# Optimization experiments

Measured on AMD Instinct MI355X. Metric: run time of the kernel, lower is better.

The kernel has to match this reference:

```python
import jax, jax.numpy as jnp
import numpy as np

NUM_EXPERTS_PER_TOK = 2

def setup_inputs() -> dict:
    key = jax.random.key(0)
    k1, k2, k3, k4 = jax.random.split(key, 4)
    B, S, D, O, E = 2, 4096, 2048, 2048, 8
    x = jax.random.normal(k1, (B, S, D), dtype=jnp.float32)
    gate_w = jax.random.normal(k2, (E, D), dtype=jnp.float32) * 0.02
    expert_w = jax.random.normal(k3, (E, O, D), dtype=jnp.float32) * 0.02
    expert_b = jax.random.normal(k4, (E, O), dtype=jnp.float32) * 0.02
    return {"x": x, "gate_w": gate_w, "expert_w": expert_w, "expert_b": expert_b}

def reference(x, gate_w, expert_w, expert_b):
    E = gate_w.shape[0]
    O = expert_w.shape[1]
    # Router: gate logits [B,S,E], top-k selection, softmax over the k logits (fp32 then cast)
    gate_logits = jnp.einsum('bsd,ed->bse', x, gate_w)
    topk_vals, topk_idx = jax.lax.top_k(gate_logits, NUM_EXPERTS_PER_TOK)
    weights = jax.nn.softmax(topk_vals.astype(jnp.float32), axis=-1).astype(x.dtype)
    # Dense combine weights [B,S,E]: weight of expert e for each token (0 if not selected)
    dense_w = jnp.sum(jax.nn.one_hot(topk_idx, E, dtype=x.dtype) * weights[..., None], axis=2)
    # Per-expert linear + weighted combine (loop over small fixed E)
    out = jnp.zeros(x.shape[:2] + (O,), dtype=x.dtype)
    for e in range(E):
        y_e = jnp.einsum('bsd,od->bso', x, expert_w[e]) + expert_b[e]
        out = out + dense_w[..., e:e + 1] * y_e
    return out
```

## Files before the change

kernel.cpp:

```cpp
#include <hip/hip_runtime.h>
#include <stdint.h>
#include <math.h>

#define T_TOK 8192
#define DIM   2048
#define OUTD  2048
#define NEXP  8

typedef __bf16 bf16x8 __attribute__((ext_vector_type(8)));
typedef float  f32x4  __attribute__((ext_vector_type(4)));

__device__ __forceinline__ unsigned short f2bf(float f) {
  union { float f; uint32_t u; } c = {f};
  uint32_t r = (c.u + 0x7FFFu + ((c.u >> 16) & 1u)) >> 16;
  return (unsigned short)r;
}
__device__ __forceinline__ float bf2f(unsigned short h) {
  union { uint32_t u; float f; } c = {((uint32_t)h) << 16};
  return c.f;
}

__device__ __forceinline__ void gld_lds16(const void* g, void* l) {
  auto gp = reinterpret_cast<const __attribute__((address_space(1))) char*>(
      reinterpret_cast<uintptr_t>(g));
  auto lp = reinterpret_cast<__attribute__((address_space(3))) char*>(
      reinterpret_cast<uintptr_t>(l));
  __builtin_amdgcn_global_load_lds(gp, lp, 16, 0, 0);
}

__global__ __launch_bounds__(256) void split_hi_lo(const float* __restrict__ src,
                                                   unsigned short* __restrict__ hi,
                                                   unsigned short* __restrict__ lo,
                                                   int n4) {
  int stride = gridDim.x * blockDim.x;
  for (int i = blockIdx.x * blockDim.x + threadIdx.x; i < n4; i += stride) {
    float4 v = reinterpret_cast<const float4*>(src)[i];
    ushort4 h, l;
    h.x = f2bf(v.x); l.x = f2bf(v.x - bf2f(h.x));
    h.y = f2bf(v.y); l.y = f2bf(v.y - bf2f(h.y));
    h.z = f2bf(v.z); l.z = f2bf(v.z - bf2f(h.z));
    h.w = f2bf(v.w); l.w = f2bf(v.w - bf2f(h.w));
    reinterpret_cast<ushort4*>(hi)[i] = h;
    reinterpret_cast<ushort4*>(lo)[i] = l;
  }
}

__global__ __launch_bounds__(256) void router(const float* __restrict__ x,
                                              const float* __restrict__ gw,
                                              int* __restrict__ cnt,
                                              int* __restrict__ tok_list,
                                              float* __restrict__ tok_w) {
  const int t    = blockIdx.x * 4 + (threadIdx.x >> 6);
  const int lane = threadIdx.x & 63;
  const float4* xr = reinterpret_cast<const float4*>(x + (size_t)t * DIM);
  double acc[NEXP];
#pragma unroll
  for (int e = 0; e < NEXP; ++e) acc[e] = 0.0;
#pragma unroll
  for (int i = 0; i < DIM / (4 * 64); ++i) {
    float4 xv = xr[i * 64 + lane];
#pragma unroll
    for (int e = 0; e < NEXP; ++e) {
      float4 gv = reinterpret_cast<const float4*>(gw + e * DIM)[i * 64 + lane];
      acc[e] += (double)xv.x * gv.x + (double)xv.y * gv.y +
                (double)xv.z * gv.z + (double)xv.w * gv.w;
    }
  }
#pragma unroll
  for (int off = 32; off >= 1; off >>= 1)
#pragma unroll
    for (int e = 0; e < NEXP; ++e) acc[e] += __shfl_down(acc[e], off, 64);
  if (lane == 0) {
    float lg[NEXP];
#pragma unroll
    for (int e = 0; e < NEXP; ++e) lg[e] = (float)acc[e];
    int i0 = 0; float v0 = lg[0];
    int i1 = -1; float v1 = -3.4e38f;
#pragma unroll
    for (int e = 1; e < NEXP; ++e) {
      if (lg[e] > v0)      { i1 = i0; v1 = v0; i0 = e; v0 = lg[e]; }
      else if (lg[e] > v1) { i1 = e;  v1 = lg[e]; }
    }
    float p  = expf(v1 - v0);
    float w0 = 1.0f / (1.0f + p);
    float w1 = p * w0;
    int s0 = atomicAdd(&cnt[i0], 1);
    tok_list[i0 * T_TOK + s0] = t; tok_w[i0 * T_TOK + s0] = w0;
    int s1 = atomicAdd(&cnt[i1], 1);
    tok_list[i1 * T_TOK + s1] = t; tok_w[i1 * T_TOK + s1] = w1;
  }
}

__global__ __launch_bounds__(256, 2) void moe_gemm(
    const unsigned short* __restrict__ xh, const unsigned short* __restrict__ xl,
    const unsigned short* __restrict__ wh, const unsigned short* __restrict__ wl,
    const float* __restrict__ eb,
    const int* __restrict__ cnt,
    const int* __restrict__ tok_list, const float* __restrict__ tok_w,
    float* __restrict__ out) {
  const int e  = blockIdx.z;
  const int ce = cnt[e];
  const int bx = blockIdx.x;
  if (bx * 128 >= ce) return;
  const int by  = blockIdx.y;
  const int tid = threadIdx.x;
  const int l   = tid & 63;
  const int w   = tid >> 6;
  const int wr  = w >> 1, wc = w & 1;

  extern __shared__ char smem[];

  int* stok = reinterpret_cast<int*>(smem);
  if (tid < 128) {
    int rg = bx * 128 + tid;
    stok[tid] = (rg < ce) ? tok_list[e * T_TOK + rg] : 0;
  }
  __syncthreads();

  size_t aOff[4], bOff[4];
  int    lOff[4];
#pragma unroll
  for (int i = 0; i < 4; ++i) {
    int g = i * 256 + tid;
    int r = g >> 3, p = g & 7, s = p ^ (r & 7);
    aOff[i] = (size_t)stok[r] * DIM + s * 8;
    bOff[i] = ((size_t)e * OUTD + by * 128 + r) * DIM + s * 8;
    lOff[i] = g * 16;
  }
  __syncthreads();

  const int rA = wr * 64 + (l & 15);
  const int rB = wc * 64 + (l & 15);
  const int p0 = ((l >> 4) + 0) ^ (l & 7);
  const int p1 = ((l >> 4) + 4) ^ (l & 7);
  const int a0 = rA * 128 + p0 * 16, a1 = rA * 128 + p1 * 16;
  const int b0 = rB * 128 + p0 * 16, b1 = rB * 128 + p1 * 16;

  f32x4 acc[4][4] = {};

  for (int kt = 0; kt < DIM / 64; ++kt) {
    const int kk = kt * 64;
#pragma unroll
    for (int i = 0; i < 4; ++i) {
      gld_lds16(xh + aOff[i] + kk, smem +         lOff[i]);
      gld_lds16(xl + aOff[i] + kk, smem + 16384 + lOff[i]);
      gld_lds16(wh + bOff[i] + kk, smem + 32768 + lOff[i]);
      gld_lds16(wl + bOff[i] + kk, smem + 49152 + lOff[i]);
    }
    asm volatile("s_waitcnt vmcnt(0)" ::: "memory");
    __syncthreads();

#pragma unroll
    for (int ks = 0; ks < 2; ++ks) {
      const int aB = ks ? a1 : a0;
      const int bB = ks ? b1 : b0;
      bf16x8 ah[4], al[4];
#pragma unroll
      for (int m = 0; m < 4; ++m) {
        ah[m] = *reinterpret_cast<const bf16x8*>(smem +         aB + m * 2048);
        al[m] = *reinterpret_cast<const bf16x8*>(smem + 16384 + aB + m * 2048);
      }
#pragma unroll
      for (int n = 0; n < 4; ++n) {
        bf16x8 bh = *reinterpret_cast<const bf16x8*>(smem + 32768 + bB + n * 2048);
        bf16x8 bl = *reinterpret_cast<const bf16x8*>(smem + 49152 + bB + n * 2048);
#pragma unroll
        for (int m = 0; m < 4; ++m) {
          acc[m][n] = __builtin_amdgcn_mfma_f32_16x16x32_bf16(ah[m], bh, acc[m][n], 0, 0, 0);
          acc[m][n] = __builtin_amdgcn_mfma_f32_16x16x32_bf16(ah[m], bl, acc[m][n], 0, 0, 0);
          acc[m][n] = __builtin_amdgcn_mfma_f32_16x16x32_bf16(al[m], bh, acc[m][n], 0, 0, 0);
        }
      }
    }
    __syncthreads();
  }

  int   tk[16];
  float wt[16];
  const int q4 = (l >> 4) * 4;
#pragma unroll
  for (int m = 0; m < 4; ++m)
#pragma unroll
    for (int q = 0; q < 4; ++q) {
      int r  = wr * 64 + m * 16 + q4 + q;
      int rg = bx * 128 + r;
      bool v = rg < ce;
      tk[m * 4 + q] = v ? tok_list[e * T_TOK + rg] : 0;
      wt[m * 4 + q] = v ? tok_w[e * T_TOK + rg] : 0.0f;
    }
#pragma unroll
  for (int n = 0; n < 4; ++n) {
    const int gc = by * 128 + wc * 64 + n * 16 + (l & 15);
    const float bias = eb[e * OUTD + gc];
#pragma unroll
    for (int m = 0; m < 4; ++m)
#pragma unroll
      for (int q = 0; q < 4; ++q) {
        float val = wt[m * 4 + q] * (acc[m][n][q] + bias);
        atomicAdd(out + (size_t)tk[m * 4 + q] * OUTD + gc, val);
      }
  }
}

extern "C" void kernel_launch(void* const* d_in, const int* in_sizes, int n_in,
                              void* d_out, int out_size, void* d_ws, size_t ws_size,
                              hipStream_t stream) {
  const float* x  = (const float*)d_in[0];
  const float* gw = (const float*)d_in[1];
  const float* ew = (const float*)d_in[2];
  const float* eb = (const float*)d_in[3];
  float* out = (float*)d_out;

  char* ws = (char*)d_ws;
  int*   cnt      = (int*)(ws);
  int*   tok_list = (int*)(ws + 256);
  float* tok_w    = (float*)(ws + 256 + 262144);
  unsigned short* xh = (unsigned short*)(ws + 524544);
  unsigned short* xl = xh + 16777216;
  unsigned short* wh = xl + 16777216;
  unsigned short* wl = wh + 33554432;

  hipMemsetAsync(cnt, 0, 256, stream);
  hipMemsetAsync(d_out, 0, (size_t)out_size * sizeof(float), stream);

  split_hi_lo<<<4096, 256, 0, stream>>>(x,  xh, xl, 16777216 / 4);
  split_hi_lo<<<4096, 256, 0, stream>>>(ew, wh, wl, 33554432 / 4);
  router<<<T_TOK / 4, 256, 0, stream>>>(x, gw, cnt, tok_list, tok_w);

  moe_gemm<<<dim3(64, 16, 8), 256, 65536, stream>>>(xh, xl, wh, wl, eb, cnt,
                                                    tok_list, tok_w, out);
}
```

Before: 1.260 ms.

## Double-buffer MoE GEMM with 256x256 tiles and fuse x split into router

Fuses the hi/lo bf16 split of x into the router kernel so x is read once instead of twice. Restructures the expert GEMM to 512-thread blocks on 256x256 output tiles with a 32-wide K step and double-buffered LDS (133 KB), issuing the next stage's global->LDS loads before computing the current one. Token ids and weights are cached in LDS for the epilogue. The larger tile improves data reuse and the prefetch overlaps memory with MFMA, but it raises LDS and register pressure, likely limits occupancy to one block per CU, and pads more rows for experts with ragged token counts.

```diff
diff --git a/kernel.cpp b/kernel.cpp
--- a/kernel.cpp
+++ b/kernel.cpp
@@ -6,6 +6,7 @@
 #define DIM   2048
 #define OUTD  2048
 #define NEXP  8
+#define NKT   (DIM / 32)
 
 typedef __bf16 bf16x8 __attribute__((ext_vector_type(8)));
 typedef float  f32x4  __attribute__((ext_vector_type(4)));
@@ -45,20 +46,31 @@
   }
 }
 
-__global__ __launch_bounds__(256) void router(const float* __restrict__ x,
-                                              const float* __restrict__ gw,
-                                              int* __restrict__ cnt,
-                                              int* __restrict__ tok_list,
-                                              float* __restrict__ tok_w) {
+__global__ __launch_bounds__(256) void router_split(const float* __restrict__ x,
+                                                    const float* __restrict__ gw,
+                                                    unsigned short* __restrict__ xh,
+                                                    unsigned short* __restrict__ xl,
+                                                    int* __restrict__ cnt,
+                                                    int* __restrict__ tok_list,
+                                                    float* __restrict__ tok_w) {
   const int t    = blockIdx.x * 4 + (threadIdx.x >> 6);
   const int lane = threadIdx.x & 63;
   const float4* xr = reinterpret_cast<const float4*>(x + (size_t)t * DIM);
+  ushort4* xhr = reinterpret_cast<ushort4*>(xh + (size_t)t * DIM);
+  ushort4* xlr = reinterpret_cast<ushort4*>(xl + (size_t)t * DIM);
   double acc[NEXP];
 #pragma unroll
   for (int e = 0; e < NEXP; ++e) acc[e] = 0.0;
 #pragma unroll
   for (int i = 0; i < DIM / (4 * 64); ++i) {
     float4 xv = xr[i * 64 + lane];
+    ushort4 h, l;
+    h.x = f2bf(xv.x); l.x = f2bf(xv.x - bf2f(h.x));
+    h.y = f2bf(xv.y); l.y = f2bf(xv.y - bf2f(h.y));
+    h.z = f2bf(xv.z); l.z = f2bf(xv.z - bf2f(h.z));
+    h.w = f2bf(xv.w); l.w = f2bf(xv.w - bf2f(h.w));
+    xhr[i * 64 + lane] = h;
+    xlr[i * 64 + lane] = l;
 #pragma unroll
     for (int e = 0; e < NEXP; ++e) {
       float4 gv = reinterpret_cast<const float4*>(gw + e * DIM)[i * 64 + lane];
@@ -91,7 +103,7 @@
   }
 }
 
-__global__ __launch_bounds__(256, 2) void moe_gemm(
+__global__ __launch_bounds__(512, 2) void moe_gemm(
     const unsigned short* __restrict__ xh, const unsigned short* __restrict__ xl,
     const unsigned short* __restrict__ wh, const unsigned short* __restrict__ wl,
     const float* __restrict__ eb,
@@ -101,105 +113,104 @@
   const int e  = blockIdx.z;
   const int ce = cnt[e];
   const int bx = blockIdx.x;
-  if (bx * 128 >= ce) return;
+  if (bx * 256 >= ce) return;
   const int by  = blockIdx.y;
   const int tid = threadIdx.x;
   const int l   = tid & 63;
   const int w   = tid >> 6;
-  const int wr  = w >> 1, wc = w & 1;
+  const int wr  = w >> 2, wc = w & 3;
 
   extern __shared__ char smem[];
-
-  int* stok = reinterpret_cast<int*>(smem);
-  if (tid < 128) {
-    int rg = bx * 128 + tid;
-    stok[tid] = (rg < ce) ? tok_list[e * T_TOK + rg] : 0;
+  int*   stok = reinterpret_cast<int*>(smem + 131072);
+  float* sw   = reinterpret_cast<float*>(smem + 132096);
+
+  if (tid < 256) {
+    int rg = bx * 256 + tid;
+    bool v = rg < ce;
+    stok[tid] = v ? tok_list[e * T_TOK + rg] : 0;
+    sw[tid]   = v ? tok_w[e * T_TOK + rg]   : 0.0f;
   }
   __syncthreads();
 
-  size_t aOff[4], bOff[4];
-  int    lOff[4];
+  const unsigned short* asrc[4];
+  const unsigned short* bsrc[4];
 #pragma unroll
   for (int i = 0; i < 4; ++i) {
-    int g = i * 256 + tid;
+    int g = i * 512 + tid;
     int r = g >> 3, p = g & 7, s = p ^ (r & 7);
-    aOff[i] = (size_t)stok[r] * DIM + s * 8;
-    bOff[i] = ((size_t)e * OUTD + by * 128 + r) * DIM + s * 8;
-    lOff[i] = g * 16;
-  }
+    asrc[i] = (s < 4 ? xh : xl) + (size_t)stok[r] * DIM + (s & 3) * 8;
+    bsrc[i] = (s < 4 ? wh : wl) + ((size_t)e * OUTD + by * 256 + r) * DIM + (s & 3) * 8;
+  }
+
+  const int ph = (l >> 4) ^ (l & 7);
+  const int pl = ((l >> 4) + 4) ^ (l & 7);
+  const int aOh = (wr * 128 + (l & 15)) * 128 + ph * 16;
+  const int aOl = (wr * 128 + (l & 15)) * 128 + pl * 16;
+  const int bOh = 32768 + (wc * 64 + (l & 15)) * 128 + ph * 16;
+  const int bOl = 32768 + (wc * 64 + (l & 15)) * 128 + pl * 16;
+
+  f32x4 acc[8][4] = {};
+
+  auto STAGE = [&](int buf, int kk) {
+    char* base = smem + buf * 65536;
+#pragma unroll
+    for (int i = 0; i < 4; ++i) {
+      gld_lds16(asrc[i] + kk, base + tid * 16 + i * 8192);
+      gld_lds16(bsrc[i] + kk, base + 32768 + tid * 16 + i * 8192);
+    }
+  };
+
+  STAGE(0, 0);
+  asm volatile("s_waitcnt vmcnt(0)" ::: "memory");
   __syncthreads();
 
-  const int rA = wr * 64 + (l & 15);
-  const int rB = wc * 64 + (l & 15);
-  const int p0 = ((l >> 4) + 0) ^ (l & 7);
-  const int p1 = ((l >> 4) + 4) ^ (l & 7);
-  const int a0 = rA * 128 + p0 * 16, a1 = rA * 128 + p1 * 16;
-  const int b0 = rB * 128 + p0 * 16, b1 = rB * 128 + p1 * 16;
-
-  f32x4 acc[4][4] = {};
-
-  for (int kt = 0; kt < DIM / 64; ++kt) {
-    const int kk = kt * 64;
-#pragma unroll
-    for (int i = 0; i < 4; ++i) {
-      gld_lds16(xh + aOff[i] + kk, smem +         lOff[i]);
-      gld_lds16(xl + aOff[i] + kk, smem + 16384 + lOff[i]);
-      gld_lds16(wh + bOff[i] + kk, smem + 32768 + lOff[i]);
-      gld_lds16(wl + bOff[i] + kk, smem + 49152 + lOff[i]);
+  for (int kt = 0; kt < NKT; ++kt) {
+    const int cur = kt & 1;
+    if (kt + 1 < NKT) STAGE(cur ^ 1, (kt + 1) * 32);
+
+    char* b = smem + cur * 65536;
+    bf16x8 bh[4], bl[4];
+#pragma unroll
+    for (int n = 0; n < 4; ++n) {
+      bh[n] = *reinterpret_cast<const bf16x8*>(b + bOh + n * 2048);
+      bl[n] = *reinterpret_cast<const bf16x8*>(b + bOl + n * 2048);
+    }
+#pragma unroll
+    for (int m = 0; m < 8; ++m) {
+      bf16x8 ah = *reinterpret_cast<const bf16x8*>(b + aOh + m * 2048);
+      bf16x8 al = *reinterpret_cast<const bf16x8*>(b + aOl + m * 2048);
+#pragma unroll
+      for (int n = 0; n < 4; ++n) {
+        acc[m][n] = __builtin_amdgcn_mfma_f32_16x16x32_bf16(ah, bh[n], acc[m][n], 0, 0, 0);
+        acc[m][n] = __builtin_amdgcn_mfma_f32_16x16x32_bf16(ah, bl[n], acc[m][n], 0, 0, 0);
+        acc[m][n] = __builtin_amdgcn_mfma_f32_16x16x32_bf16(al, bh[n], acc[m][n], 0, 0, 0);
+      }
     }
     asm volatile("s_waitcnt vmcnt(0)" ::: "memory");
     __syncthreads();
-
-#pragma unroll
-    for (int ks = 0; ks < 2; ++ks) {
-      const int aB = ks ? a1 : a0;
-      const int bB = ks ? b1 : b0;
-      bf16x8 ah[4], al[4];
-#pragma unroll
-      for (int m = 0; m < 4; ++m) {
-        ah[m] = *reinterpret_cast<const bf16x8*>(smem +         aB + m * 2048);
-        al[m] = *reinterpret_cast<const bf16x8*>(smem + 16384 + aB + m * 2048);
+  }
+
+#pragma unroll
+  for (int n = 0; n < 4; ++n) {
+    const int gc = by * 256 + wc * 64 + n * 16 + (l & 15);
+    const float bias = eb[e * OUTD + gc];
+#pragma unroll
+    for (int m = 0; m < 8; ++m) {
+      const int r = wr * 128 + m * 16 + (l >> 4) * 4;
+#pragma unroll
+      for (int q = 0; q < 4; ++q) {
+        int   tk = stok[r + q];
+        float wt = sw[r + q];
+        float val = wt * (acc[m][n][q] + bias);
+        atomicAdd(out + (size_t)tk * OUTD + gc, val);
       }
-#pragma unroll
-      for (int n = 0; n < 4; ++n) {
-        bf16x8 bh = *reinterpret_cast<const bf16x8*>(smem + 32768 + bB + n * 2048);
-        bf16x8 bl = *reinterpret_cast<const bf16x8*>(smem + 49152 + bB + n * 2048);
-#pragma unroll
-        for (int m = 0; m < 4; ++m) {
-          acc[m][n] = __builtin_amdgcn_mfma_f32_16x16x32_bf16(ah[m], bh, acc[m][n], 0, 0, 0);
-          acc[m][n] = __builtin_amdgcn_mfma_f32_16x16x32_bf16(ah[m], bl, acc[m][n], 0, 0, 0);
-          acc[m][n] = __builtin_amdgcn_mfma_f32_16x16x32_bf16(al[m], bh, acc[m][n], 0, 0, 0);
-        }
-      }
-    }
-    __syncthreads();
-  }
-
-  int   tk[16];
-  float wt[16];
-  const int q4 = (l >> 4) * 4;
-#pragma unroll
-  for (int m = 0; m < 4; ++m)
-#pragma unroll
-    for (int q = 0; q < 4; ++q) {
-      int r  = wr * 64 + m * 16 + q4 + q;
-      int rg = bx * 128 + r;
-      bool v = rg < ce;
-      tk[m * 4 + q] = v ? tok_list[e * T_TOK + rg] : 0;
-      wt[m * 4 + q] = v ? tok_w[e * T_TOK + rg] : 0.0f;
-    }
-#pragma unroll
-  for (int n = 0; n < 4; ++n) {
-    const int gc = by * 128 + wc * 64 + n * 16 + (l & 15);
-    const float bias = eb[e * OUTD + gc];
-#pragma unroll
-    for (int m = 0; m < 4; ++m)
-#pragma unroll
-      for (int q = 0; q < 4; ++q) {
-        float val = wt[m * 4 + q] * (acc[m][n][q] + bias);
-        atomicAdd(out + (size_t)tk[m * 4 + q] * OUTD + gc, val);
-      }
-  }
+    }
+  }
+}
+
+__attribute__((constructor)) static void set_lds_attr() {
+  hipFuncSetAttribute((const void*)moe_gemm,
+                      hipFuncAttributeMaxDynamicSharedMemorySize, 133120);
 }
 
 extern "C" void kernel_launch(void* const* d_in, const int* in_sizes, int n_in,
@@ -223,10 +234,9 @@
   hipMemsetAsync(cnt, 0, 256, stream);
   hipMemsetAsync(d_out, 0, (size_t)out_size * sizeof(float), stream);
 
-  split_hi_lo<<<4096, 256, 0, stream>>>(x,  xh, xl, 16777216 / 4);
   split_hi_lo<<<4096, 256, 0, stream>>>(ew, wh, wl, 33554432 / 4);
-  router<<<T_TOK / 4, 256, 0, stream>>>(x, gw, cnt, tok_list, tok_w);
-
-  moe_gemm<<<dim3(64, 16, 8), 256, 65536, stream>>>(xh, xl, wh, wl, eb, cnt,
+  router_split<<<T_TOK / 4, 256, 0, stream>>>(x, gw, xh, xl, cnt, tok_list, tok_w);
+
+  moe_gemm<<<dim3(32, 8, 8), 512, 133120, stream>>>(xh, xl, wh, wl, eb, cnt,
                                                     tok_list, tok_w, out);
 }
```

After: 1.687 ms. 1.34x slower.
